# Optimization experiments

Hardware: AMD Instinct MI355X
Metric: run time of the kernel (lower is better)

The kernel has to match this reference:

```python
import jax, jax.numpy as jnp
import numpy as np

SQRT2 = float(np.sqrt(2.0))

# near_sym_b biort filters (13,19)-tap, as used by DTCWT level 1
_H0O = np.array([-0.0017578, 0.0, 0.0222656, -0.046875, -0.0482422, 0.296875,
                 0.5554688, 0.296875, -0.0482422, -0.046875, 0.0222656, 0.0,
                 -0.0017578], np.float32)
_H1O = np.array([-0.0000706, 0.0, 0.0013419, -0.0018834, -0.0071568, 0.023856,
                 0.0556431, -0.0516881, -0.2997576, 0.5594308, -0.2997576,
                 -0.0516881, 0.0556431, 0.023856, -0.0071568, -0.0018834,
                 0.0013419, 0.0, -0.0000706], np.float32)

def _sgn(L):
    return np.where((np.arange(L) - L // 2) % 2 == 0, 1.0, -1.0).astype(np.float32)

# synthesis filters: G0(z)=H1(-z), G1(z)=-H0(-z) (zero-phase centered)
_G0O = _H1O * _sgn(19)
_G1O = -(_H0O * _sgn(13))


def _filt(x, h, axis):
    # separable symmetric-extension FIR filter along H (axis=2) or W (axis=3)
    L = int(h.shape[0]); m = L // 2
    pad = [(0, 0)] * 4
    pad[axis] = (m, m)
    xp = jnp.pad(x, pad, mode='symmetric')
    k = h.reshape((1, 1, L, 1)) if axis == 2 else h.reshape((1, 1, 1, L))
    B, C = x.shape[0], x.shape[1]
    y = jax.lax.conv_general_dilated(
        xp.reshape((B * C, 1) + xp.shape[2:]), k,
        window_strides=(1, 1), padding='VALID',
        dimension_numbers=('NCHW', 'OIHW', 'NCHW'))
    return y.reshape(x.shape)


def _q2c(y):
    # quad pixels -> two complex subimages
    y = y * (1.0 / SQRT2)
    a = y[..., 0::2, 0::2]; b = y[..., 0::2, 1::2]
    c = y[..., 1::2, 0::2]; d = y[..., 1::2, 1::2]
    return (a - d, b + c), (a + d, b - c)


def _c2q(w1r, w1i, w2r, w2i):
    B, C, H2, W2 = w1r.shape
    top = jnp.stack([w1r + w2r, w1i + w2i], axis=-1).reshape(B, C, H2, 2 * W2)
    bot = jnp.stack([w1i - w2i, w2r - w1r], axis=-1).reshape(B, C, H2, 2 * W2)
    return jnp.stack([top, bot], axis=-2).reshape(B, C, 2 * H2, 2 * W2) * (1.0 / SQRT2)


def _dtcwt_fwd(x, h0, h1):
    lo = _filt(x, h0, 3); hi = _filt(x, h1, 3)
    ll = _filt(lo, h0, 2)
    lh = _filt(lo, h1, 2); hl = _filt(hi, h0, 2); hh = _filt(hi, h1, 2)
    lhp, lhq = _q2c(lh); hlp, hlq = _q2c(hl); hhp, hhq = _q2c(hh)
    bands = [lhp, hhp, hlp, hlq, hhq, lhq]  # 15,45,75,105,135,165 degrees
    reals = jnp.stack([b[0] for b in bands], axis=2)
    imags = jnp.stack([b[1] for b in bands], axis=2)
    return ll, jnp.stack([reals, imags], axis=-1)  # (B,C,H,W), (B,C,6,H/2,W/2,2)


def _dtcwt_inv(ll, yh, g0, g1):
    r, im = yh[..., 0], yh[..., 1]
    lh = _c2q(r[:, :, 0], im[:, :, 0], r[:, :, 5], im[:, :, 5])
    hl = _c2q(r[:, :, 2], im[:, :, 2], r[:, :, 3], im[:, :, 3])
    hh = _c2q(r[:, :, 1], im[:, :, 1], r[:, :, 4], im[:, :, 4])
    lo = _filt(ll, g0, 2) + _filt(lh, g1, 2)
    hi = _filt(hl, g0, 2) + _filt(hh, g1, 2)
    return _filt(lo, g0, 3) + _filt(hi, g1, 3)


def _dwconv(x, w, b):
    y = jax.lax.conv_general_dilated(
        x, w, window_strides=(1, 1), padding='SAME',
        feature_group_count=w.shape[0],
        dimension_numbers=('NCHW', 'OIHW', 'NCHW'))
    return y + b[None, :, None, None]


def _forward(x, conv_w, conv_b, w_ll, w_lh1, w_lh2, b_lh1, b_lh2,
             w_t1, w_t2, b_t1, b_t2, H, W):
    B, N, C = x.shape
    Ch = C // 2
    xi_ = x.reshape(B, H, W, C).transpose(0, 3, 1, 2)  # (B,C,H,W)
    x1, x2 = xi_[:, :Ch], xi_[:, Ch:]
    x1 = _dwconv(x1, conv_w, conv_b)
    h0 = jnp.asarray(_H0O); h1 = jnp.asarray(_H1O)
    xl, xh = _dtcwt_fwd(x2, h0, h1)
    xl = xl * w_ll
    H2, W2 = H // 2, W // 2
    nb = 4; bs = Ch // nb
    mul = lambda t, w: jnp.einsum('...bd,bdk->...bk', t, w)
    # channel mixing: block-diagonal complex MLP over channel blocks
    xp = jnp.transpose(xh, (5, 0, 2, 3, 4, 1)).reshape(2, B, 6, H2, W2, nb, bs)
    xr, xim = xp[0], xp[1]
    xr1 = jax.nn.relu(mul(xr, w_lh1[0]) - mul(xim, w_lh1[1]) + b_lh1[0])
    xi1 = jax.nn.relu(mul(xr, w_lh1[1]) + mul(xim, w_lh1[0]) + b_lh1[1])
    xr2 = mul(xr1, w_lh2[0]) - mul(xi1, w_lh2[1]) + b_lh2[0]
    xi2 = mul(xr1, w_lh2[1]) + mul(xi1, w_lh2[0]) + b_lh2[1]
    cm = jnp.stack([xr2, xi2], -1).reshape(B, 6, H2, W2, Ch, 2)
    t = jnp.transpose(cm, (5, 0, 4, 1, 2, 3))  # (2,B,Ch,6,H2,W2)
    tr, ti = t[0], t[1]
    tr1 = jax.nn.relu(mul(tr, w_t1[0]) - mul(ti, w_t1[1]) + b_t1[0])
    ti1 = jax.nn.relu(mul(tr, w_t1[1]) + mul(ti, w_t1[0]) + b_t1[1])
    tr2 = mul(tr1, w_t2[0]) - mul(ti1, w_t2[1]) + b_t2[0]
    ti2 = mul(tr1, w_t2[1]) + mul(ti1, w_t2[0]) + b_t2[1]
    yh = jnp.stack([tr2, ti2], -1)  # (B,Ch,6,H2,W2,2)
    x2r = _dtcwt_inv(xl, yh, jnp.asarray(_G0O), jnp.asarray(_G1O))
    out = jnp.concatenate([x1, x2r], axis=1)
    return out.transpose(0, 2, 3, 1).reshape(B, N, C)


def setup_inputs() -> dict:
    key = jax.random.key(0)
    ks = jax.random.split(key, 12)
    B, H, W, C = 256, 28, 28, 128
    Ch = C // 2
    nb, bs, tb = 4, Ch // 4, 14
    return {
        'x': jax.random.normal(ks[0], (B, H * W, C), jnp.float32),
        'conv_w': jax.random.normal(ks[1], (Ch, 1, 3, 3), jnp.float32) * 0.1,
        'conv_b': jnp.zeros((Ch,), jnp.float32),
        'w_ll': jax.random.normal(ks[2], (Ch, H, W), jnp.float32) * 0.02,
        'w_lh1': jax.random.normal(ks[3], (2, nb, bs, bs), jnp.float32) * 0.02,
        'w_lh2': jax.random.normal(ks[4], (2, nb, bs, bs), jnp.float32) * 0.02,
        'b_lh1': jax.random.normal(ks[5], (2, nb, bs), jnp.float32) * 0.02,
        'b_lh2': jax.random.normal(ks[6], (2, nb, bs), jnp.float32) * 0.02,
        'w_t1': jax.random.normal(ks[7], (2, tb, tb, tb), jnp.float32) * 0.02,
        'w_t2': jax.random.normal(ks[8], (2, tb, tb, tb), jnp.float32) * 0.02,
        'b_t1': jax.random.normal(ks[9], (2, tb, tb), jnp.float32) * 0.02,
        'b_t2': jax.random.normal(ks[10], (2, tb, tb), jnp.float32) * 0.02,
        'H': H, 'W': W,
    }


def reference(x, conv_w, conv_b, w_ll, w_lh1, w_lh2, b_lh1, b_lh2,
              w_t1, w_t2, b_t1, b_t2, H, W):
    return _forward(x, conv_w, conv_b, w_ll, w_lh1, w_lh2, b_lh1, b_lh2,
                    w_t1, w_t2, b_t1, b_t2, H, W)
```

## Files before the change

kernel.cpp:

```cpp
#include <hip/hip_runtime.h>


#define DI __device__ __forceinline__

__device__ constexpr float F_H0[13] = {
  -0.0017578f, 0.0f, 0.0222656f, -0.046875f, -0.0482422f, 0.296875f,
   0.5554688f, 0.296875f, -0.0482422f, -0.046875f, 0.0222656f, 0.0f, -0.0017578f};
__device__ constexpr float F_H1[19] = {
  -7.06e-05f, 0.0f, 0.0013419f, -0.0018834f, -0.0071568f, 0.023856f,
   0.0556431f, -0.0516881f, -0.2997576f, 0.5594308f, -0.2997576f, -0.0516881f,
   0.0556431f, 0.023856f, -0.0071568f, -0.0018834f, 0.0013419f, 0.0f, -7.06e-05f};
__device__ constexpr float F_G0[19] = {
   7.06e-05f, 0.0f, -0.0013419f, -0.0018834f, 0.0071568f, 0.023856f,
  -0.0556431f, -0.0516881f, 0.2997576f, 0.5594308f, 0.2997576f, -0.0516881f,
  -0.0556431f, 0.023856f, 0.0071568f, -0.0018834f, -0.0013419f, 0.0f, 7.06e-05f};
__device__ constexpr float F_G1[13] = {
   0.0017578f, 0.0f, -0.0222656f, -0.046875f, 0.0482422f, 0.296875f,
  -0.5554688f, 0.296875f, 0.0482422f, -0.046875f, -0.0222656f, 0.0f, 0.0017578f};

DI constexpr int refl28(int i) { return i < 0 ? -1 - i : (i >= 28 ? 55 - i : i); }

#define S2C 0.70710678118654752f

__global__ __launch_bounds__(256) void k_dwconv(const float* __restrict__ x,
    const float* __restrict__ cw, const float* __restrict__ cb,
    float* __restrict__ out) {
  int tid = blockIdx.x * 256 + threadIdx.x;
  int c = tid & 63;
  int s = tid >> 6;
  int w = s % 28; int t2 = s / 28; int h = t2 % 28;
  const float* k = cw + c * 9;
  const float* xb = x + (size_t)s * 128 + c;
  float acc = cb[c];
  bool hm = h > 0, hp = h < 27, wm = w > 0, wp = w < 27;
  if (hm) {
    const float* r = xb - 28 * 128;
    if (wm) acc = fmaf(r[-128], k[0], acc);
    acc = fmaf(r[0], k[1], acc);
    if (wp) acc = fmaf(r[128], k[2], acc);
  }
  if (wm) acc = fmaf(xb[-128], k[3], acc);
  acc = fmaf(xb[0], k[4], acc);
  if (wp) acc = fmaf(xb[128], k[5], acc);
  if (hp) {
    const float* r = xb + 28 * 128;
    if (wm) acc = fmaf(r[-128], k[6], acc);
    acc = fmaf(r[0], k[7], acc);
    if (wp) acc = fmaf(r[128], k[8], acc);
  }
  out[(size_t)s * 128 + c] = acc;
}

__global__ __launch_bounds__(256) void k_rowfilt(const float* __restrict__ x,
    float* __restrict__ lo, float* __restrict__ hi) {
  int tid = threadIdx.x;
  int c = tid & 63;
  int line = blockIdx.x * 4 + (tid >> 6);
  const float* xp = x + (size_t)line * 28 * 128 + 64 + c;
  float v[28];
#pragma unroll
  for (int w = 0; w < 28; w++) v[w] = xp[w * 128];
  float* lp = lo + (size_t)line * 28 * 64 + c;
  float* hp = hi + (size_t)line * 28 * 64 + c;
#pragma unroll
  for (int w = 0; w < 28; w++) {
    float aLo = 0.f, aHi = 0.f;
#pragma unroll
    for (int t = 0; t < 13; t++) aLo = fmaf(F_H0[t], v[refl28(w - 6 + t)], aLo);
#pragma unroll
    for (int t = 0; t < 19; t++) aHi = fmaf(F_H1[t], v[refl28(w - 9 + t)], aHi);
    lp[w * 64] = aLo;
    hp[w * 64] = aHi;
  }
}

__global__ __launch_bounds__(256) void k_colfilt(const float* __restrict__ lo,
    const float* __restrict__ hi, const float* __restrict__ wll,
    float* __restrict__ xl, float* __restrict__ xhr, float* __restrict__ xhi) {
  __shared__ float swll[3584];
  int tid = threadIdx.x;
  int w2 = blockIdx.x >> 6;
  for (int j = tid; j < 3584; j += 256) {
    int cc = j & 63, t = j >> 6;
    int h = t >> 1, woff = t & 1;
    swll[j] = wll[cc * 784 + h * 28 + 2 * w2 + woff];
  }
  __syncthreads();
  int c = tid & 63;
  int unit = blockIdx.x * 4 + (tid >> 6);
  int b = unit & 255;
  const int hs = 28 * 64;
  int base_in = (b * 784 + 2 * w2) * 64 + c;
  float v0[28], v1[28];
#pragma unroll
  for (int h = 0; h < 28; h++) {
    v0[h] = lo[base_in + h * hs];
    v1[h] = lo[base_in + h * hs + 64];
  }
#pragma unroll
  for (int h = 0; h < 28; h++) {
    float a0 = 0.f, a1 = 0.f;
#pragma unroll
    for (int t = 0; t < 13; t++) {
      a0 = fmaf(F_H0[t], v0[refl28(h - 6 + t)], a0);
      a1 = fmaf(F_H0[t], v1[refl28(h - 6 + t)], a1);
    }
    int o = (b * 784 + h * 28 + 2 * w2) * 64 + c;
    xl[o]      = a0 * swll[(h * 2 + 0) * 64 + c];
    xl[o + 64] = a1 * swll[(h * 2 + 1) * 64 + c];
  }
  {
    float e0[28], e1[28];
#pragma unroll
    for (int h = 0; h < 28; h++) {
      float a0 = 0.f, a1 = 0.f;
#pragma unroll
      for (int t = 0; t < 19; t++) {
        a0 = fmaf(F_H1[t], v0[refl28(h - 9 + t)], a0);
        a1 = fmaf(F_H1[t], v1[refl28(h - 9 + t)], a1);
      }
      e0[h] = a0; e1[h] = a1;
    }
    int bb = (b * 6 * 196 + w2) * 64 + c;
#pragma unroll
    for (int i = 0; i < 14; i++) {
      float A = e0[2 * i], Bv = e1[2 * i], C = e0[2 * i + 1], D = e1[2 * i + 1];
      xhr[bb + 0 * 12544 + i * 896] = (A - D) * S2C;
      xhi[bb + 0 * 12544 + i * 896] = (Bv + C) * S2C;
      xhr[bb + 5 * 12544 + i * 896] = (A + D) * S2C;
      xhi[bb + 5 * 12544 + i * 896] = (Bv - C) * S2C;
    }
  }
#pragma unroll
  for (int h = 0; h < 28; h++) {
    v0[h] = hi[base_in + h * hs];
    v1[h] = hi[base_in + h * hs + 64];
  }
  {
    float e0[28], e1[28];
#pragma unroll
    for (int h = 0; h < 28; h++) {
      float a0 = 0.f, a1 = 0.f;
#pragma unroll
      for (int t = 0; t < 13; t++) {
        a0 = fmaf(F_H0[t], v0[refl28(h - 6 + t)], a0);
        a1 = fmaf(F_H0[t], v1[refl28(h - 6 + t)], a1);
      }
      e0[h] = a0; e1[h] = a1;
    }
    int bb = (b * 6 * 196 + w2) * 64 + c;
#pragma unroll
    for (int i = 0; i < 14; i++) {
      float A = e0[2 * i], Bv = e1[2 * i], C = e0[2 * i + 1], D = e1[2 * i + 1];
      xhr[bb + 2 * 12544 + i * 896] = (A - D) * S2C;
      xhi[bb + 2 * 12544 + i * 896] = (Bv + C) * S2C;
      xhr[bb + 3 * 12544 + i * 896] = (A + D) * S2C;
      xhi[bb + 3 * 12544 + i * 896] = (Bv - C) * S2C;
    }
  }
  {
    float e0[28], e1[28];
#pragma unroll
    for (int h = 0; h < 28; h++) {
      float a0 = 0.f, a1 = 0.f;
#pragma unroll
      for (int t = 0; t < 19; t++) {
        a0 = fmaf(F_H1[t], v0[refl28(h - 9 + t)], a0);
        a1 = fmaf(F_H1[t], v1[refl28(h - 9 + t)], a1);
      }
      e0[h] = a0; e1[h] = a1;
    }
    int bb = (b * 6 * 196 + w2) * 64 + c;
#pragma unroll
    for (int i = 0; i < 14; i++) {
      float A = e0[2 * i], Bv = e1[2 * i], C = e0[2 * i + 1], D = e1[2 * i + 1];
      xhr[bb + 1 * 12544 + i * 896] = (A - D) * S2C;
      xhi[bb + 1 * 12544 + i * 896] = (Bv + C) * S2C;
      xhr[bb + 4 * 12544 + i * 896] = (A + D) * S2C;
      xhi[bb + 4 * 12544 + i * 896] = (Bv - C) * S2C;
    }
  }
}

__global__ __launch_bounds__(256) void k_chmix(float* __restrict__ xhr,
    float* __restrict__ xhi,
    const float* __restrict__ w1, const float* __restrict__ w2,
    const float* __restrict__ b1, const float* __restrict__ b2) {
  __shared__ __align__(16) float sw1[2048];
  __shared__ __align__(16) float sw2[2048];
  __shared__ __align__(16) float sb1[128];
  __shared__ __align__(16) float sb2[128];
  int tid = threadIdx.x;
  for (int i = tid; i < 1024; i += 256) {
    int dk = i >> 2, blk = i & 3;
    int li = dk * 8 + blk * 2;
    sw1[li]     = w1[blk * 256 + dk];
    sw1[li + 1] = w1[1024 + blk * 256 + dk];
    sw2[li]     = w2[blk * 256 + dk];
    sw2[li + 1] = w2[1024 + blk * 256 + dk];
  }
  if (tid < 64) {
    int k = tid >> 2, blk = tid & 3;
    int li = k * 8 + blk * 2;
    sb1[li] = b1[blk * 16 + k]; sb1[li + 1] = b1[64 + blk * 16 + k];
    sb2[li] = b2[blk * 16 + k]; sb2[li + 1] = b2[64 + blk * 16 + k];
  }
  __syncthreads();
  int idx = blockIdx.x * 256 + tid;
  int blk = idx & 3;
  int p = idx >> 2;
  size_t base = (size_t)p * 64 + blk * 16;
  float xr[16], xi[16];
  const float4* pr = (const float4*)(xhr + base);
  const float4* pi = (const float4*)(xhi + base);
#pragma unroll
  for (int j = 0; j < 4; j++) {
    float4 a = pr[j];
    xr[4 * j] = a.x; xr[4 * j + 1] = a.y; xr[4 * j + 2] = a.z; xr[4 * j + 3] = a.w;
    float4 bb = pi[j];
    xi[4 * j] = bb.x; xi[4 * j + 1] = bb.y; xi[4 * j + 2] = bb.z; xi[4 * j + 3] = bb.w;
  }
  int wb = blk * 2;
  float yr[16], yi[16];
#pragma unroll
  for (int k = 0; k < 16; k++) {
    float2 bv = *(const float2*)(sb1 + k * 8 + wb);
    float ar = bv.x, ai = bv.y;
#pragma unroll
    for (int d = 0; d < 16; d++) {
      float2 wv = *(const float2*)(sw1 + (d * 16 + k) * 8 + wb);
      ar = fmaf(xr[d], wv.x, ar); ar = fmaf(-xi[d], wv.y, ar);
      ai = fmaf(xr[d], wv.y, ai); ai = fmaf(xi[d], wv.x, ai);
    }
    yr[k] = fmaxf(ar, 0.f); yi[k] = fmaxf(ai, 0.f);
  }
#pragma unroll
  for (int k = 0; k < 16; k++) {
    float2 bv = *(const float2*)(sb2 + k * 8 + wb);
    float ar = bv.x, ai = bv.y;
#pragma unroll
    for (int d = 0; d < 16; d++) {
      float2 wv = *(const float2*)(sw2 + (d * 16 + k) * 8 + wb);
      ar = fmaf(yr[d], wv.x, ar); ar = fmaf(-yi[d], wv.y, ar);
      ai = fmaf(yr[d], wv.y, ai); ai = fmaf(yi[d], wv.x, ai);
    }
    xr[k] = ar; xi[k] = ai;
  }
  float4* qr = (float4*)(xhr + base);
  float4* qi = (float4*)(xhi + base);
#pragma unroll
  for (int j = 0; j < 4; j++) {
    qr[j] = make_float4(xr[4 * j], xr[4 * j + 1], xr[4 * j + 2], xr[4 * j + 3]);
    qi[j] = make_float4(xi[4 * j], xi[4 * j + 1], xi[4 * j + 2], xi[4 * j + 3]);
  }
}

__global__ __launch_bounds__(256) void k_tokmix(float* __restrict__ xhr,
    float* __restrict__ xhi,
    const float* __restrict__ wt1, const float* __restrict__ wt2,
    const float* __restrict__ bt1, const float* __restrict__ bt2) {
  __shared__ __align__(16) float st1[5488];
  __shared__ __align__(16) float st2[5488];
  __shared__ __align__(16) float sB1[392];
  __shared__ __align__(16) float sB2[392];
  int tid = threadIdx.x;
  for (int i = tid; i < 2744; i += 256) {
    st1[2 * i] = wt1[i]; st1[2 * i + 1] = wt1[2744 + i];
    st2[2 * i] = wt2[i]; st2[2 * i + 1] = wt2[2744 + i];
  }
  for (int i = tid; i < 196; i += 256) {
    sB1[2 * i] = bt1[i]; sB1[2 * i + 1] = bt1[196 + i];
    sB2[2 * i] = bt2[i]; sB2[2 * i + 1] = bt2[196 + i];
  }
  __syncthreads();
  int idx = blockIdx.x * 256 + tid;
  int c = idx & 63;
  int pp = idx >> 6;
  int h2 = pp % 14;
  int baseA = pp * 896 + c;
  int baseB = (pp + 10752) * 896 + c;
  float trA[14], tiA[14], trB[14], tiB[14];
#pragma unroll
  for (int d = 0; d < 14; d++) {
    trA[d] = xhr[baseA + d * 64]; tiA[d] = xhi[baseA + d * 64];
    trB[d] = xhr[baseB + d * 64]; tiB[d] = xhi[baseB + d * 64];
  }
  const float* w1 = st1 + h2 * 392;
  const float* w2 = st2 + h2 * 392;
  const float* bb1 = sB1 + h2 * 28;
  const float* bb2 = sB2 + h2 * 28;
  float mrA[14], miA[14], mrB[14], miB[14];
#pragma unroll
  for (int k = 0; k < 14; k++) {
    float br = bb1[2 * k], bi = bb1[2 * k + 1];
    float arA = br, aiA = bi, arB = br, aiB = bi;
#pragma unroll
    for (int d = 0; d < 14; d++) {
      float wr = w1[(d * 14 + k) * 2], wi = w1[(d * 14 + k) * 2 + 1];
      arA = fmaf(trA[d], wr, arA); arA = fmaf(-tiA[d], wi, arA);
      aiA = fmaf(trA[d], wi, aiA); aiA = fmaf(tiA[d], wr, aiA);
      arB = fmaf(trB[d], wr, arB); arB = fmaf(-tiB[d], wi, arB);
      aiB = fmaf(trB[d], wi, aiB); aiB = fmaf(tiB[d], wr, aiB);
    }
    mrA[k] = fmaxf(arA, 0.f); miA[k] = fmaxf(aiA, 0.f);
    mrB[k] = fmaxf(arB, 0.f); miB[k] = fmaxf(aiB, 0.f);
  }
#pragma unroll
  for (int k = 0; k < 14; k++) {
    float br = bb2[2 * k], bi = bb2[2 * k + 1];
    float arA = br, aiA = bi, arB = br, aiB = bi;
#pragma unroll
    for (int d = 0; d < 14; d++) {
      float wr = w2[(d * 14 + k) * 2], wi = w2[(d * 14 + k) * 2 + 1];
      arA = fmaf(mrA[d], wr, arA); arA = fmaf(-miA[d], wi, arA);
      aiA = fmaf(mrA[d], wi, aiA); aiA = fmaf(miA[d], wr, aiA);
      arB = fmaf(mrB[d], wr, arB); arB = fmaf(-miB[d], wi, arB);
      aiB = fmaf(mrB[d], wi, aiB); aiB = fmaf(miB[d], wr, aiB);
    }
    xhr[baseA + k * 64] = arA; xhi[baseA + k * 64] = aiA;
    xhr[baseB + k * 64] = arB; xhi[baseB + k * 64] = aiB;
  }
}

__global__ __launch_bounds__(256) void k_invcol(const float* __restrict__ xl,
    const float* __restrict__ xhr, const float* __restrict__ xhi,
    float* __restrict__ lo2, float* __restrict__ hi2) {
  int tid = threadIdx.x;
  int c = tid & 63;
  int line = blockIdx.x * 4 + (tid >> 6);
  int w = line % 28, b = line / 28;
  int w2 = w >> 1, pw = w & 1;
  const int hs = 28 * 64;
  int sp = (b * 784 + w) * 64 + c;
  int bb = (b * 6 * 196 + w2) * 64 + c;
  {
    float xlv[28], lhf[28];
#pragma unroll
    for (int h = 0; h < 28; h++) xlv[h] = xl[sp + h * hs];
    const float* p0r = xhr + bb + 0 * 12544;
    const float* p0i = xhi + bb + 0 * 12544;
    const float* p5r = xhr + bb + 5 * 12544;
    const float* p5i = xhi + bb + 5 * 12544;
#pragma unroll
    for (int i = 0; i < 14; i++) {
      float y0r = p0r[i * 896], y0i = p0i[i * 896];
      float y5r = p5r[i * 896], y5i = p5i[i * 896];
      float top, bot;
      if (pw) { top = y0i + y5i; bot = y5r - y0r; }
      else    { top = y0r + y5r; bot = y0i - y5i; }
      lhf[2 * i] = top * S2C; lhf[2 * i + 1] = bot * S2C;
    }
#pragma unroll
    for (int h = 0; h < 28; h++) {
      float acc = 0.f;
#pragma unroll
      for (int t = 0; t < 19; t++) acc = fmaf(F_G0[t], xlv[refl28(h - 9 + t)], acc);
#pragma unroll
      for (int t = 0; t < 13; t++) acc = fmaf(F_G1[t], lhf[refl28(h - 6 + t)], acc);
      lo2[sp + h * hs] = acc;
    }
  }
  {
    float hlC[28], hhD[28];
    const float* p2r = xhr + bb + 2 * 12544;
    const float* p2i = xhi + bb + 2 * 12544;
    const float* p3r = xhr + bb + 3 * 12544;
    const float* p3i = xhi + bb + 3 * 12544;
#pragma unroll
    for (int i = 0; i < 14; i++) {
      float y0r = p2r[i * 896], y0i = p2i[i * 896];
      float y5r = p3r[i * 896], y5i = p3i[i * 896];
      float top, bot;
      if (pw) { top = y0i + y5i; bot = y5r - y0r; }
      else    { top = y0r + y5r; bot = y0i - y5i; }
      hlC[2 * i] = top * S2C; hlC[2 * i + 1] = bot * S2C;
    }
    const float* p1r = xhr + bb + 1 * 12544;
    const float* p1i = xhi + bb + 1 * 12544;
    const float* p4r = xhr + bb + 4 * 12544;
    const float* p4i = xhi + bb + 4 * 12544;
#pragma unroll
    for (int i = 0; i < 14; i++) {
      float y0r = p1r[i * 896], y0i = p1i[i * 896];
      float y5r = p4r[i * 896], y5i = p4i[i * 896];
      float top, bot;
      if (pw) { top = y0i + y5i; bot = y5r - y0r; }
      else    { top = y0r + y5r; bot = y0i - y5i; }
      hhD[2 * i] = top * S2C; hhD[2 * i + 1] = bot * S2C;
    }
#pragma unroll
    for (int h = 0; h < 28; h++) {
      float acc = 0.f;
#pragma unroll
      for (int t = 0; t < 19; t++) acc = fmaf(F_G0[t], hlC[refl28(h - 9 + t)], acc);
#pragma unroll
      for (int t = 0; t < 13; t++) acc = fmaf(F_G1[t], hhD[refl28(h - 6 + t)], acc);
      hi2[sp + h * hs] = acc;
    }
  }
}

__global__ __launch_bounds__(256) void k_invrow(const float* __restrict__ lo2,
    const float* __restrict__ hi2, float* __restrict__ out) {
  int tid = threadIdx.x;
  int c = tid & 63;
  int line = blockIdx.x * 4 + (tid >> 6);
  const float* lr = lo2 + (size_t)line * 28 * 64 + c;
  const float* hr = hi2 + (size_t)line * 28 * 64 + c;
  float vl[28], vh[28];
#pragma unroll
  for (int w = 0; w < 28; w++) { vl[w] = lr[w * 64]; vh[w] = hr[w * 64]; }
  float* op = out + (size_t)line * 28 * 128 + 64 + c;
#pragma unroll
  for (int w = 0; w < 28; w++) {
    float acc = 0.f;
#pragma unroll
    for (int t = 0; t < 19; t++) acc = fmaf(F_G0[t], vl[refl28(w - 9 + t)], acc);
#pragma unroll
    for (int t = 0; t < 13; t++) acc = fmaf(F_G1[t], vh[refl28(w - 6 + t)], acc);
    op[w * 128] = acc;
  }
}

extern "C" void kernel_launch(void* const* d_in, const int* in_sizes, int n_in,
                              void* d_out, int out_size, void* d_ws, size_t ws_size,
                              hipStream_t stream) {
  const float* x    = (const float*)d_in[0];
  const float* cw   = (const float*)d_in[1];
  const float* cb   = (const float*)d_in[2];
  const float* wll  = (const float*)d_in[3];
  const float* wlh1 = (const float*)d_in[4];
  const float* wlh2 = (const float*)d_in[5];
  const float* blh1 = (const float*)d_in[6];
  const float* blh2 = (const float*)d_in[7];
  const float* wt1  = (const float*)d_in[8];
  const float* wt2  = (const float*)d_in[9];
  const float* bt1  = (const float*)d_in[10];
  const float* bt2  = (const float*)d_in[11];
  float* out = (float*)d_out;
  float* ws = (float*)d_ws;

  const size_t NSP = (size_t)256 * 784 * 64;
  const size_t NXH = (size_t)256 * 6 * 196 * 64;
  float* lo  = ws;
  float* hi  = lo + NSP;
  float* xl  = hi + NSP;
  float* xhr = xl + NSP;
  float* xhi = xhr + NXH;

  dim3 blk(256);
  k_dwconv <<<50176, blk, 0, stream>>>(x, cw, cb, out);
  k_rowfilt<<<1792,  blk, 0, stream>>>(x, lo, hi);
  k_colfilt<<<896,   blk, 0, stream>>>(lo, hi, wll, xl, xhr, xhi);
  k_chmix  <<<4704,  blk, 0, stream>>>(xhr, xhi, wlh1, wlh2, blh1, blh2);
  k_tokmix <<<2688,  blk, 0, stream>>>(xhr, xhi, wt1, wt2, bt1, bt2);
  k_invcol <<<1792,  blk, 0, stream>>>(xl, xhr, xhi, lo, hi);
  k_invrow <<<1792,  blk, 0, stream>>>(lo, hi, out);
  (void)in_sizes; (void)n_in; (void)out_size; (void)ws_size;
}
```

Measured before the change: 694.4 us.

## Load mixing weights as wave-uniform scalar loads instead of staging in LDS

Both the channel-mix and token-mix kernels stop copying their weight and bias tables into shared memory at block start. The thread mapping is changed so that the weight-block or row index is uniform across each wavefront (readfirstlane), which lets weights be read straight from global memory through the scalar cache. The loops are reordered to be outer-product style, with each input element broadcast into accumulators. This removes the per-block LDS fill, the barrier and the LDS reads, but raises register pressure and relies on the compiler actually emitting scalar loads.

```diff
diff --git a/kernel.cpp b/kernel.cpp
--- a/kernel.cpp
+++ b/kernel.cpp
@@ -186,72 +186,91 @@
     float* __restrict__ xhi,
     const float* __restrict__ w1, const float* __restrict__ w2,
     const float* __restrict__ b1, const float* __restrict__ b2) {
-  __shared__ __align__(16) float sw1[2048];
-  __shared__ __align__(16) float sw2[2048];
-  __shared__ __align__(16) float sb1[128];
-  __shared__ __align__(16) float sb2[128];
-  int tid = threadIdx.x;
-  for (int i = tid; i < 1024; i += 256) {
-    int dk = i >> 2, blk = i & 3;
-    int li = dk * 8 + blk * 2;
-    sw1[li]     = w1[blk * 256 + dk];
-    sw1[li + 1] = w1[1024 + blk * 256 + dk];
-    sw2[li]     = w2[blk * 256 + dk];
-    sw2[li + 1] = w2[1024 + blk * 256 + dk];
-  }
-  if (tid < 64) {
-    int k = tid >> 2, blk = tid & 3;
-    int li = k * 8 + blk * 2;
-    sb1[li] = b1[blk * 16 + k]; sb1[li + 1] = b1[64 + blk * 16 + k];
-    sb2[li] = b2[blk * 16 + k]; sb2[li + 1] = b2[64 + blk * 16 + k];
-  }
-  __syncthreads();
-  int idx = blockIdx.x * 256 + tid;
-  int blk = idx & 3;
-  int p = idx >> 2;
+  int tid = threadIdx.x;
+  int lane = tid & 63;
+  int blk = __builtin_amdgcn_readfirstlane(tid >> 6);
+  int p = blockIdx.x * 64 + lane;
   size_t base = (size_t)p * 64 + blk * 16;
   float xr[16], xi[16];
-  const float4* pr = (const float4*)(xhr + base);
-  const float4* pi = (const float4*)(xhi + base);
-#pragma unroll
-  for (int j = 0; j < 4; j++) {
-    float4 a = pr[j];
-    xr[4 * j] = a.x; xr[4 * j + 1] = a.y; xr[4 * j + 2] = a.z; xr[4 * j + 3] = a.w;
-    float4 bb = pi[j];
-    xi[4 * j] = bb.x; xi[4 * j + 1] = bb.y; xi[4 * j + 2] = bb.z; xi[4 * j + 3] = bb.w;
-  }
-  int wb = blk * 2;
-  float yr[16], yi[16];
-#pragma unroll
-  for (int k = 0; k < 16; k++) {
-    float2 bv = *(const float2*)(sb1 + k * 8 + wb);
-    float ar = bv.x, ai = bv.y;
+  {
+    const float4* pr = (const float4*)(xhr + base);
+    const float4* pi4 = (const float4*)(xhi + base);
+#pragma unroll
+    for (int j = 0; j < 4; j++) {
+      float4 a = pr[j];
+      xr[4 * j] = a.x; xr[4 * j + 1] = a.y; xr[4 * j + 2] = a.z; xr[4 * j + 3] = a.w;
+      float4 bq = pi4[j];
+      xi[4 * j] = bq.x; xi[4 * j + 1] = bq.y; xi[4 * j + 2] = bq.z; xi[4 * j + 3] = bq.w;
+    }
+  }
+  float ar[16], ai[16];
+  {
+    const float4* br4 = (const float4*)(b1 + blk * 16);
+    const float4* bi4 = (const float4*)(b1 + 64 + blk * 16);
+#pragma unroll
+    for (int q = 0; q < 4; q++) {
+      float4 r = br4[q], m = bi4[q];
+      ar[4 * q] = r.x; ar[4 * q + 1] = r.y; ar[4 * q + 2] = r.z; ar[4 * q + 3] = r.w;
+      ai[4 * q] = m.x; ai[4 * q + 1] = m.y; ai[4 * q + 2] = m.z; ai[4 * q + 3] = m.w;
+    }
 #pragma unroll
     for (int d = 0; d < 16; d++) {
-      float2 wv = *(const float2*)(sw1 + (d * 16 + k) * 8 + wb);
-      ar = fmaf(xr[d], wv.x, ar); ar = fmaf(-xi[d], wv.y, ar);
-      ai = fmaf(xr[d], wv.y, ai); ai = fmaf(xi[d], wv.x, ai);
-    }
-    yr[k] = fmaxf(ar, 0.f); yi[k] = fmaxf(ai, 0.f);
-  }
-#pragma unroll
-  for (int k = 0; k < 16; k++) {
-    float2 bv = *(const float2*)(sb2 + k * 8 + wb);
-    float ar = bv.x, ai = bv.y;
+      float xdr = xr[d], xdi = xi[d];
+      const float4* wr4 = (const float4*)(w1 + blk * 256 + d * 16);
+      const float4* wi4 = (const float4*)(w1 + 1024 + blk * 256 + d * 16);
+#pragma unroll
+      for (int q = 0; q < 4; q++) {
+        float4 r = wr4[q], m = wi4[q];
+        ar[4*q+0] = fmaf(xdr, r.x, ar[4*q+0]); ar[4*q+0] = fmaf(-xdi, m.x, ar[4*q+0]);
+        ai[4*q+0] = fmaf(xdr, m.x, ai[4*q+0]); ai[4*q+0] = fmaf( xdi, r.x, ai[4*q+0]);
+        ar[4*q+1] = fmaf(xdr, r.y, ar[4*q+1]); ar[4*q+1] = fmaf(-xdi, m.y, ar[4*q+1]);
+        ai[4*q+1] = fmaf(xdr, m.y, ai[4*q+1]); ai[4*q+1] = fmaf( xdi, r.y, ai[4*q+1]);
+        ar[4*q+2] = fmaf(xdr, r.z, ar[4*q+2]); ar[4*q+2] = fmaf(-xdi, m.z, ar[4*q+2]);
+        ai[4*q+2] = fmaf(xdr, m.z, ai[4*q+2]); ai[4*q+2] = fmaf( xdi, r.z, ai[4*q+2]);
+        ar[4*q+3] = fmaf(xdr, r.w, ar[4*q+3]); ar[4*q+3] = fmaf(-xdi, m.w, ar[4*q+3]);
+        ai[4*q+3] = fmaf(xdr, m.w, ai[4*q+3]); ai[4*q+3] = fmaf( xdi, r.w, ai[4*q+3]);
+      }
+    }
+#pragma unroll
+    for (int k = 0; k < 16; k++) {
+      xr[k] = fmaxf(ar[k], 0.f);
+      xi[k] = fmaxf(ai[k], 0.f);
+    }
+  }
+  {
+    const float4* br4 = (const float4*)(b2 + blk * 16);
+    const float4* bi4 = (const float4*)(b2 + 64 + blk * 16);
+#pragma unroll
+    for (int q = 0; q < 4; q++) {
+      float4 r = br4[q], m = bi4[q];
+      ar[4 * q] = r.x; ar[4 * q + 1] = r.y; ar[4 * q + 2] = r.z; ar[4 * q + 3] = r.w;
+      ai[4 * q] = m.x; ai[4 * q + 1] = m.y; ai[4 * q + 2] = m.z; ai[4 * q + 3] = m.w;
+    }
 #pragma unroll
     for (int d = 0; d < 16; d++) {
-      float2 wv = *(const float2*)(sw2 + (d * 16 + k) * 8 + wb);
-      ar = fmaf(yr[d], wv.x, ar); ar = fmaf(-yi[d], wv.y, ar);
-      ai = fmaf(yr[d], wv.y, ai); ai = fmaf(yi[d], wv.x, ai);
-    }
-    xr[k] = ar; xi[k] = ai;
+      float xdr = xr[d], xdi = xi[d];
+      const float4* wr4 = (const float4*)(w2 + blk * 256 + d * 16);
+      const float4* wi4 = (const float4*)(w2 + 1024 + blk * 256 + d * 16);
+#pragma unroll
+      for (int q = 0; q < 4; q++) {
+        float4 r = wr4[q], m = wi4[q];
+        ar[4*q+0] = fmaf(xdr, r.x, ar[4*q+0]); ar[4*q+0] = fmaf(-xdi, m.x, ar[4*q+0]);
+        ai[4*q+0] = fmaf(xdr, m.x, ai[4*q+0]); ai[4*q+0] = fmaf( xdi, r.x, ai[4*q+0]);
+        ar[4*q+1] = fmaf(xdr, r.y, ar[4*q+1]); ar[4*q+1] = fmaf(-xdi, m.y, ar[4*q+1]);
+        ai[4*q+1] = fmaf(xdr, m.y, ai[4*q+1]); ai[4*q+1] = fmaf( xdi, r.y, ai[4*q+1]);
+        ar[4*q+2] = fmaf(xdr, r.z, ar[4*q+2]); ar[4*q+2] = fmaf(-xdi, m.z, ar[4*q+2]);
+        ai[4*q+2] = fmaf(xdr, m.z, ai[4*q+2]); ai[4*q+2] = fmaf( xdi, r.z, ai[4*q+2]);
+        ar[4*q+3] = fmaf(xdr, r.w, ar[4*q+3]); ar[4*q+3] = fmaf(-xdi, m.w, ar[4*q+3]);
+        ai[4*q+3] = fmaf(xdr, m.w, ai[4*q+3]); ai[4*q+3] = fmaf( xdi, r.w, ai[4*q+3]);
+      }
+    }
   }
   float4* qr = (float4*)(xhr + base);
   float4* qi = (float4*)(xhi + base);
 #pragma unroll
   for (int j = 0; j < 4; j++) {
-    qr[j] = make_float4(xr[4 * j], xr[4 * j + 1], xr[4 * j + 2], xr[4 * j + 3]);
-    qi[j] = make_float4(xi[4 * j], xi[4 * j + 1], xi[4 * j + 2], xi[4 * j + 3]);
+    qr[j] = make_float4(ar[4 * j], ar[4 * j + 1], ar[4 * j + 2], ar[4 * j + 3]);
+    qi[j] = make_float4(ai[4 * j], ai[4 * j + 1], ai[4 * j + 2], ai[4 * j + 3]);
   }
 }
 
@@ -259,23 +278,9 @@
     float* __restrict__ xhi,
     const float* __restrict__ wt1, const float* __restrict__ wt2,
     const float* __restrict__ bt1, const float* __restrict__ bt2) {
-  __shared__ __align__(16) float st1[5488];
-  __shared__ __align__(16) float st2[5488];
-  __shared__ __align__(16) float sB1[392];
-  __shared__ __align__(16) float sB2[392];
-  int tid = threadIdx.x;
-  for (int i = tid; i < 2744; i += 256) {
-    st1[2 * i] = wt1[i]; st1[2 * i + 1] = wt1[2744 + i];
-    st2[2 * i] = wt2[i]; st2[2 * i + 1] = wt2[2744 + i];
-  }
-  for (int i = tid; i < 196; i += 256) {
-    sB1[2 * i] = bt1[i]; sB1[2 * i + 1] = bt1[196 + i];
-    sB2[2 * i] = bt2[i]; sB2[2 * i + 1] = bt2[196 + i];
-  }
-  __syncthreads();
-  int idx = blockIdx.x * 256 + tid;
-  int c = idx & 63;
-  int pp = idx >> 6;
+  int tid = threadIdx.x;
+  int c = tid & 63;
+  int pp = __builtin_amdgcn_readfirstlane(blockIdx.x * 4 + (tid >> 6));
   int h2 = pp % 14;
   int baseA = pp * 896 + c;
   int baseB = (pp + 10752) * 896 + c;
@@ -285,40 +290,68 @@
     trA[d] = xhr[baseA + d * 64]; tiA[d] = xhi[baseA + d * 64];
     trB[d] = xhr[baseB + d * 64]; tiB[d] = xhi[baseB + d * 64];
   }
-  const float* w1 = st1 + h2 * 392;
-  const float* w2 = st2 + h2 * 392;
-  const float* bb1 = sB1 + h2 * 28;
-  const float* bb2 = sB2 + h2 * 28;
-  float mrA[14], miA[14], mrB[14], miB[14];
+  const float* W1 = wt1 + h2 * 196;
+  const float* W2 = wt2 + h2 * 196;
+  const float* B1 = bt1 + h2 * 14;
+  const float* B2 = bt2 + h2 * 14;
+  float arA[14], aiA[14], arB[14], aiB[14];
 #pragma unroll
   for (int k = 0; k < 14; k++) {
-    float br = bb1[2 * k], bi = bb1[2 * k + 1];
-    float arA = br, aiA = bi, arB = br, aiB = bi;
-#pragma unroll
-    for (int d = 0; d < 14; d++) {
-      float wr = w1[(d * 14 + k) * 2], wi = w1[(d * 14 + k) * 2 + 1];
-      arA = fmaf(trA[d], wr, arA); arA = fmaf(-tiA[d], wi, arA);
-      aiA = fmaf(trA[d], wi, aiA); aiA = fmaf(tiA[d], wr, aiA);
-      arB = fmaf(trB[d], wr, arB); arB = fmaf(-tiB[d], wi, arB);
-      aiB = fmaf(trB[d], wi, aiB); aiB = fmaf(tiB[d], wr, aiB);
-    }
-    mrA[k] = fmaxf(arA, 0.f); miA[k] = fmaxf(aiA, 0.f);
-    mrB[k] = fmaxf(arB, 0.f); miB[k] = fmaxf(aiB, 0.f);
+    float br = B1[k], bi = B1[196 + k];
+    arA[k] = br; aiA[k] = bi; arB[k] = br; aiB[k] = bi;
+  }
+#pragma unroll
+  for (int d = 0; d < 14; d++) {
+    float tAr = trA[d], tAi = tiA[d], tBr = trB[d], tBi = tiB[d];
+    const float2* r2 = (const float2*)(W1 + d * 14);
+    const float2* i2 = (const float2*)(W1 + 2744 + d * 14);
+#pragma unroll
+    for (int q = 0; q < 7; q++) {
+      float2 wr = r2[q], wi = i2[q];
+      int k = 2 * q;
+      arA[k]   = fmaf(tAr, wr.x, arA[k]);   arA[k]   = fmaf(-tAi, wi.x, arA[k]);
+      aiA[k]   = fmaf(tAr, wi.x, aiA[k]);   aiA[k]   = fmaf( tAi, wr.x, aiA[k]);
+      arB[k]   = fmaf(tBr, wr.x, arB[k]);   arB[k]   = fmaf(-tBi, wi.x, arB[k]);
+      aiB[k]   = fmaf(tBr, wi.x, aiB[k]);   aiB[k]   = fmaf( tBi, wr.x, aiB[k]);
+      arA[k+1] = fmaf(tAr, wr.y, arA[k+1]); arA[k+1] = fmaf(-tAi, wi.y, arA[k+1]);
+      aiA[k+1] = fmaf(tAr, wi.y, aiA[k+1]); aiA[k+1] = fmaf( tAi, wr.y, aiA[k+1]);
+      arB[k+1] = fmaf(tBr, wr.y, arB[k+1]); arB[k+1] = fmaf(-tBi, wi.y, arB[k+1]);
+      aiB[k+1] = fmaf(tBr, wi.y, aiB[k+1]); aiB[k+1] = fmaf( tBi, wr.y, aiB[k+1]);
+    }
   }
 #pragma unroll
   for (int k = 0; k < 14; k++) {
-    float br = bb2[2 * k], bi = bb2[2 * k + 1];
-    float arA = br, aiA = bi, arB = br, aiB = bi;
-#pragma unroll
-    for (int d = 0; d < 14; d++) {
-      float wr = w2[(d * 14 + k) * 2], wi = w2[(d * 14 + k) * 2 + 1];
-      arA = fmaf(mrA[d], wr, arA); arA = fmaf(-miA[d], wi, arA);
-      aiA = fmaf(mrA[d], wi, aiA); aiA = fmaf(miA[d], wr, aiA);
-      arB = fmaf(mrB[d], wr, arB); arB = fmaf(-miB[d], wi, arB);
-      aiB = fmaf(mrB[d], wi, aiB); aiB = fmaf(miB[d], wr, aiB);
-    }
-    xhr[baseA + k * 64] = arA; xhi[baseA + k * 64] = aiA;
-    xhr[baseB + k * 64] = arB; xhi[baseB + k * 64] = aiB;
+    trA[k] = fmaxf(arA[k], 0.f); tiA[k] = fmaxf(aiA[k], 0.f);
+    trB[k] = fmaxf(arB[k], 0.f); tiB[k] = fmaxf(aiB[k], 0.f);
+  }
+#pragma unroll
+  for (int k = 0; k < 14; k++) {
+    float br = B2[k], bi = B2[196 + k];
+    arA[k] = br; aiA[k] = bi; arB[k] = br; aiB[k] = bi;
+  }
+#pragma unroll
+  for (int d = 0; d < 14; d++) {
+    float tAr = trA[d], tAi = tiA[d], tBr = trB[d], tBi = tiB[d];
+    const float2* r2 = (const float2*)(W2 + d * 14);
+    const float2* i2 = (const float2*)(W2 + 2744 + d * 14);
+#pragma unroll
+    for (int q = 0; q < 7; q++) {
+      float2 wr = r2[q], wi = i2[q];
+      int k = 2 * q;
+      arA[k]   = fmaf(tAr, wr.x, arA[k]);   arA[k]   = fmaf(-tAi, wi.x, arA[k]);
+      aiA[k]   = fmaf(tAr, wi.x, aiA[k]);   aiA[k]   = fmaf( tAi, wr.x, aiA[k]);
+      arB[k]   = fmaf(tBr, wr.x, arB[k]);   arB[k]   = fmaf(-tBi, wi.x, arB[k]);
+      aiB[k]   = fmaf(tBr, wi.x, aiB[k]);   aiB[k]   = fmaf( tBi, wr.x, aiB[k]);
+      arA[k+1] = fmaf(tAr, wr.y, arA[k+1]); arA[k+1] = fmaf(-tAi, wi.y, arA[k+1]);
+      aiA[k+1] = fmaf(tAr, wi.y, aiA[k+1]); aiA[k+1] = fmaf( tAi, wr.y, aiA[k+1]);
+      arB[k+1] = fmaf(tBr, wr.y, arB[k+1]); arB[k+1] = fmaf(-tBi, wi.y, arB[k+1]);
+      aiB[k+1] = fmaf(tBr, wi.y, aiB[k+1]); aiB[k+1] = fmaf( tBi, wr.y, aiB[k+1]);
+    }
+  }
+#pragma unroll
+  for (int k = 0; k < 14; k++) {
+    xhr[baseA + k * 64] = arA[k]; xhi[baseA + k * 64] = aiA[k];
+    xhr[baseB + k * 64] = arB[k]; xhi[baseB + k * 64] = aiB[k];
   }
 }
 
```

Result: slower. 802.6 us (+15.6%).
